# Optimization experiments

Measured on AMD Instinct MI355X. Metric: run time of the kernel, lower is better.

## Reference

```python
import jax, jax.numpy as jnp
import numpy as np

B, S, D, H = 2, 2048, 1024, 16
DK = D // H  # 64
THETA = 10000.0


def setup_inputs() -> dict:
    key = jax.random.key(0)
    ks = jax.random.split(key, 5)
    scale = 1.0 / np.sqrt(D)
    return {
        "x": jax.random.normal(ks[0], (B, S, D), dtype=jnp.float32),
        "Wq": jax.random.normal(ks[1], (D, D), dtype=jnp.float32) * scale,
        "Wk": jax.random.normal(ks[2], (D, D), dtype=jnp.float32) * scale,
        "Wv": jax.random.normal(ks[3], (D, D), dtype=jnp.float32) * scale,
        "Wo": jax.random.normal(ks[4], (D, D), dtype=jnp.float32) * scale,
    }


def _rope(t):
    # t: (B, H, S, DK); interleaved-pair rotary embedding with positions 0..S-1
    s = t.shape[-2]
    inv_freq = 1.0 / (THETA ** (jnp.arange(0, DK, 2, dtype=jnp.float32) / DK))  # (DK/2,)
    ang = jnp.arange(s, dtype=jnp.float32)[:, None] * inv_freq[None, :]  # (S, DK/2)
    cos, sin = jnp.cos(ang), jnp.sin(ang)
    x1 = t[..., 0::2]
    x2 = t[..., 1::2]
    r1 = x1 * cos - x2 * sin
    r2 = x1 * sin + x2 * cos
    return jnp.stack([r1, r2], axis=-1).reshape(t.shape)


def reference(x, Wq, Wk, Wv, Wo):
    # Projections (Linear: y = x @ W^T), split heads -> (B, H, S, DK)
    def proj(W):
        y = jnp.einsum('bsd,ed->bse', x, W)
        return y.reshape(B, S, H, DK).transpose(0, 2, 1, 3)

    Q = _rope(proj(Wq))
    K = _rope(proj(Wk))
    V = proj(Wv)

    scores = jnp.einsum('bhqd,bhkd->bhqk', Q, K)
    scores = jnp.clip(scores, -80.0, 80.0)
    causal = jnp.tril(jnp.ones((S, S), dtype=bool))  # (S, S)
    scores = jnp.where(causal, scores, -jnp.inf)
    weights = jax.nn.softmax(scores / np.sqrt(DK), axis=-1)
    att = jnp.einsum('bhqk,bhkd->bhqd', weights, V)
    att = att.transpose(0, 2, 1, 3).reshape(B, S, D)
    return jnp.einsum('bsd,ed->bse', att, Wo)
```

## Files before the change

### kernel.cpp

```cpp
#include <hip/hip_runtime.h>
#include <hip/hip_bf16.h>

#define B_  2
#define S_  2048
#define D_  1024
#define H_  16
#define DK_ 64
#define BH_ (B_*H_)
#define M_  (B_*S_)

typedef __attribute__((ext_vector_type(8))) short bf16x8;
typedef __attribute__((ext_vector_type(4))) float f32x4;

__device__ inline float bf2f(unsigned short u) {
    return __uint_as_float(((unsigned)u) << 16);
}
__device__ inline unsigned short f2bf(float f) {
    unsigned u = __float_as_uint(f);
    u += 0x7fffu + ((u >> 16) & 1u);
    return (unsigned short)(u >> 16);
}
__device__ inline unsigned short f2bf_hw(float f) {
    __hip_bfloat16 h = __float2bfloat16(f);
    return *reinterpret_cast<unsigned short*>(&h);
}
__device__ inline unsigned packbf2(float lo, float hi) {
    return (unsigned)f2bf_hw(lo) | ((unsigned)f2bf_hw(hi) << 16);
}

__device__ inline void gld16(const void* g, void* l) {
    __builtin_amdgcn_global_load_lds(
        (const __attribute__((address_space(1))) unsigned int*)g,
        (__attribute__((address_space(3))) unsigned int*)l, 16, 0, 0);
}

__global__ void cast_f32_to_bf16(const float* __restrict__ src,
                                 unsigned short* __restrict__ dst, int n) {
    int i = (blockIdx.x * blockDim.x + threadIdx.x) * 4;
    int stride = gridDim.x * blockDim.x * 4;
    for (int j = i; j < n; j += stride) {
        float4 v = *reinterpret_cast<const float4*>(src + j);
        ushort4 o;
        o.x = f2bf(v.x); o.y = f2bf(v.y); o.z = f2bf(v.z); o.w = f2bf(v.w);
        *reinterpret_cast<ushort4*>(dst + j) = o;
    }
}

__global__ void cast4_f32_to_bf16(const float* __restrict__ s0, const float* __restrict__ s1,
                                  const float* __restrict__ s2, const float* __restrict__ s3,
                                  unsigned short* __restrict__ d0, unsigned short* __restrict__ d1,
                                  unsigned short* __restrict__ d2, unsigned short* __restrict__ d3) {
    const float* s; unsigned short* d;
    switch (blockIdx.y) {
        case 0: s = s0; d = d0; break;
        case 1: s = s1; d = d1; break;
        case 2: s = s2; d = d2; break;
        default: s = s3; d = d3; break;
    }
    int j = (blockIdx.x * blockDim.x + threadIdx.x) * 4;
    float4 v = *reinterpret_cast<const float4*>(s + j);
    ushort4 o;
    o.x = f2bf(v.x); o.y = f2bf(v.y); o.z = f2bf(v.z); o.w = f2bf(v.w);
    *reinterpret_cast<ushort4*>(d + j) = o;
}

#define BMQ 128
#define BNQ 128

__global__ __launch_bounds__(256)
void gemm_qkv(const unsigned short* __restrict__ A, const unsigned short* __restrict__ Wcat,
              unsigned short* __restrict__ Qf, unsigned short* __restrict__ Kf,
              unsigned short* __restrict__ Vf) {
    __shared__ unsigned short As[BMQ * 64];
    __shared__ unsigned short Bs[BNQ * 64];
    const int K = D_;
    const int tid  = threadIdx.x;
    const int lane = tid & 63;
    const int wid  = tid >> 6;
    const int wm = wid & 1, wn = wid >> 1;
    const int m0 = blockIdx.y * BMQ, n0 = blockIdx.x * BNQ;
    const int g  = lane >> 4, cl = lane & 15;

    f32x4 acc[4][4];
#pragma unroll
    for (int i = 0; i < 4; i++)
#pragma unroll
        for (int j = 0; j < 4; j++) acc[i][j] = f32x4{0.f, 0.f, 0.f, 0.f};

    const int srow = tid >> 3;
    const unsigned short* Asrc[4];
    const unsigned short* Bsrc[4];
#pragma unroll
    for (int q = 0; q < 4; q++) {
        int row = srow + q * 32;
        Asrc[q] = A    + (long)(m0 + row) * K + (((tid & 7) ^ (srow & 7)) * 8);
        Bsrc[q] = Wcat + (long)(n0 + row) * K + (((tid & 7) ^ (srow & 7)) * 8);
    }

    for (int k0 = 0; k0 < K; k0 += 64) {
        __syncthreads();
#pragma unroll
        for (int q = 0; q < 4; q++) gld16(Asrc[q] + k0, As + tid * 8 + q * 2048);
#pragma unroll
        for (int q = 0; q < 4; q++) gld16(Bsrc[q] + k0, Bs + tid * 8 + q * 2048);
        __syncthreads();

#pragma unroll
        for (int kk = 0; kk < 2; kk++) {
            bf16x8 af[4], bfr[4];
#pragma unroll
            for (int i = 0; i < 4; i++) {
                int row = wm*64 + i*16 + cl;
                af[i]  = *reinterpret_cast<const bf16x8*>(As + row * 64 + (((kk*4 + g) ^ (cl & 7)) * 8));
            }
#pragma unroll
            for (int j = 0; j < 4; j++) {
                int row = wn*64 + j*16 + cl;
                bfr[j] = *reinterpret_cast<const bf16x8*>(Bs + row * 64 + (((kk*4 + g) ^ (cl & 7)) * 8));
            }
#pragma unroll
            for (int i = 0; i < 4; i++)
#pragma unroll
                for (int j = 0; j < 4; j++)
                    acc[i][j] = __builtin_amdgcn_mfma_f32_16x16x32_bf16(af[i], bfr[j], acc[i][j], 0, 0, 0);
        }
    }

    const int mat = n0 >> 10;
    if (mat < 2) {
        float invf[4];
#pragma unroll
        for (int jj = 0; jj < 4; jj++)
            invf[jj] = exp2f(-(float)(jj*8 + (cl >> 1)) * 0.4152410118569779f);
#pragma unroll
        for (int i = 0; i < 4; i++) {
#pragma unroll
            for (int jj = 0; jj < 4; jj++) {
                const int gcl = (n0 & 1023) + wn*64 + jj*16 + cl;
                const int hh = gcl >> 6;
                const int dk = jj*16 + cl;
#pragma unroll
                for (int rr = 0; rr < 4; rr++) {
                    int gr = m0 + wm*64 + i*16 + g*4 + rr;
                    int bb = gr >> 11, s = gr & (S_ - 1);
                    float v = acc[i][jj][rr];
                    float p = __shfl_xor(v, 1);
                    float ang = (float)s * invf[jj];
                    float sn = __sinf(ang), cs = __cosf(ang);
                    float r = (cl & 1) ? fmaf(v, cs, p * sn) : fmaf(v, cs, -p * sn);
                    long idx;
                    if (mat == 0) {
                        const int lane_p = (s & 15) | (((dk >> 3) & 3) << 4);
                        idx = ((long)(bb*H_ + hh) * 128 + (s >> 4)) * 1024
                            + (dk >> 5) * 512 + lane_p * 8 + (dk & 7);
                        Qf[idx] = f2bf_hw(r);
                    } else {
                        const int vv = s & 63;
                        const int ng = ((vv >> 5) << 1) | ((vv >> 2) & 1);
                        const int slot = ((vv & 31) >> 3) * 4 + (vv & 3);
                        const int lane_p = slot | (((dk >> 3) & 3) << 4);
                        idx = (((long)(bb*H_ + hh) * 32 + (s >> 6)) * 4 + ng) * 1024
                            + (dk >> 5) * 512 + lane_p * 8 + (dk & 7);
                        Kf[idx] = f2bf_hw(r);
                    }
                }
            }
        }
    } else {
#pragma unroll
        for (int i = 0; i < 4; i++) {
#pragma unroll
            for (int jj = 0; jj < 4; jj++) {
                const int gcl = (n0 & 1023) + wn*64 + jj*16 + cl;
                const int hh = gcl >> 6;
                const int sbase = m0 + wm*64 + i*16 + g*4;
                const int bb = sbase >> 11, s0l = sbase & (S_ - 1);
                const int lane_p = cl | (((s0l >> 3) & 3) << 4);
                const int e0 = s0l & 7;
                ushort4 o;
                o.x = f2bf_hw(acc[i][jj][0]); o.y = f2bf_hw(acc[i][jj][1]);
                o.z = f2bf_hw(acc[i][jj][2]); o.w = f2bf_hw(acc[i][jj][3]);
                long idx = ((long)(bb*H_ + hh) * 4 + jj) * 32768
                         + (long)(s0l >> 5) * 512 + lane_p * 8 + e0;
                *reinterpret_cast<ushort4*>(Vf + idx) = o;
            }
        }
    }
}

#define BM 64
#define BN 128

__global__ __launch_bounds__(256)
void gemm_out(const unsigned short* __restrict__ A, const unsigned short* __restrict__ Bw,
              float* __restrict__ Cf) {
    __shared__ unsigned short As[BM * 64];
    __shared__ unsigned short Bs[BN * 64];
    const int K = D_;
    const int tid  = threadIdx.x;
    const int lane = tid & 63;
    const int wid  = tid >> 6;
    const int wm = wid & 1, wn = wid >> 1;
    const int m0 = blockIdx.y * BM, n0 = blockIdx.x * BN;
    const int g  = lane >> 4, cl = lane & 15;

    f32x4 acc[2][4];
#pragma unroll
    for (int i = 0; i < 2; i++)
#pragma unroll
        for (int j = 0; j < 4; j++) acc[i][j] = f32x4{0.f, 0.f, 0.f, 0.f};

    const int srow = tid >> 3;
    const unsigned short* Asrc[2];
    const unsigned short* Bsrc[4];
#pragma unroll
    for (int q = 0; q < 2; q++) {
        int row = srow + q * 32;
        Asrc[q] = A + (long)(m0 + row) * K + (((tid & 7) ^ (srow & 7)) * 8);
    }
#pragma unroll
    for (int q = 0; q < 4; q++) {
        int row = srow + q * 32;
        Bsrc[q] = Bw + (long)(n0 + row) * K + (((tid & 7) ^ (srow & 7)) * 8);
    }

    for (int k0 = 0; k0 < K; k0 += 64) {
        __syncthreads();
#pragma unroll
        for (int q = 0; q < 2; q++) gld16(Asrc[q] + k0, As + tid * 8 + q * 2048);
#pragma unroll
        for (int q = 0; q < 4; q++) gld16(Bsrc[q] + k0, Bs + tid * 8 + q * 2048);
        __syncthreads();

#pragma unroll
        for (int kk = 0; kk < 2; kk++) {
            bf16x8 af[2], bfr[4];
#pragma unroll
            for (int i = 0; i < 2; i++) {
                int row = wm*32 + i*16 + cl;
                af[i]  = *reinterpret_cast<const bf16x8*>(As + row * 64 + (((kk*4 + g) ^ (cl & 7)) * 8));
            }
#pragma unroll
            for (int j = 0; j < 4; j++) {
                int row = wn*64 + j*16 + cl;
                bfr[j] = *reinterpret_cast<const bf16x8*>(Bs + row * 64 + (((kk*4 + g) ^ (cl & 7)) * 8));
            }
#pragma unroll
            for (int i = 0; i < 2; i++)
#pragma unroll
                for (int j = 0; j < 4; j++)
                    acc[i][j] = __builtin_amdgcn_mfma_f32_16x16x32_bf16(af[i], bfr[j], acc[i][j], 0, 0, 0);
        }
    }

#pragma unroll
    for (int i = 0; i < 2; i++)
#pragma unroll
        for (int j = 0; j < 4; j++)
#pragma unroll
            for (int rr = 0; rr < 4; rr++) {
                int gr = m0 + wm*32 + i*16 + g*4 + rr;
                int gc = n0 + wn*64 + j*16 + cl;
                Cf[(long)gr * D_ + gc] = acc[i][j][rr];
            }
}

#define WQ    32
#define KVBLK 64

__global__ __launch_bounds__(256)
void flash_attn(const unsigned short* __restrict__ Qf, const unsigned short* __restrict__ Kf,
                const unsigned short* __restrict__ Vf, unsigned short* __restrict__ Att) {
    __shared__ __align__(16) char smem[17408];
    const int tid  = threadIdx.x;
    const int lane = tid & 63;
    const int wid  = tid >> 6;
    const int g = lane >> 4, cl = lane & 15;
    const int bh = blockIdx.x & (BH_ - 1);
    const int pr = blockIdx.x >> 5;
    const int b = bh >> 4, h = bh & (H_ - 1);

    f32x4* Ol = reinterpret_cast<f32x4*>(smem);
    float* Ll = reinterpret_cast<float*>(smem + 16384);

    const unsigned short* Qb = Qf + (long)bh * 131072;
    const unsigned short* Kb = Kf + (long)bh * 131072;
    const unsigned short* Vb = Vf + (long)bh * 131072;

    const float RS = 0.125f * 1.44269504f;
    const float RB = -10.f * 1.44269504f;

    for (int half = 0; half < 2; half++) {
        const int qt = half ? (S_/WQ - 1 - pr) : pr;
        const int q0 = qt * WQ;
        const int nt = (q0 + WQ + KVBLK - 1) / KVBLK;

        bf16x8 aq[2][2];
#pragma unroll
        for (int m = 0; m < 2; m++)
#pragma unroll
            for (int c = 0; c < 2; c++)
                aq[m][c] = *reinterpret_cast<const bf16x8*>(Qb + ((q0 >> 4) + m) * 1024 + c * 512 + lane * 8);

        f32x4 o[2][4];
#pragma unroll
        for (int m = 0; m < 2; m++)
#pragma unroll
            for (int t = 0; t < 4; t++) o[m][t] = f32x4{0.f, 0.f, 0.f, 0.f};
        float lp[2] = {0.f, 0.f};

        for (int j = wid; j < nt; j += 4) {
            const int kv0 = j * KVBLK;
            bf16x8 bk[4][2];
#pragma unroll
            for (int n = 0; n < 4; n++)
#pragma unroll
                for (int c = 0; c < 2; c++)
                    bk[n][c] = *reinterpret_cast<const bf16x8*>(Kb + (j * 4 + n) * 1024 + c * 512 + lane * 8);
            f32x4 sc[2][4];
#pragma unroll
            for (int m = 0; m < 2; m++)
#pragma unroll
                for (int n = 0; n < 4; n++) {
                    f32x4 z = f32x4{0.f, 0.f, 0.f, 0.f};
                    z = __builtin_amdgcn_mfma_f32_16x16x32_bf16(bk[n][0], aq[m][0], z, 0, 0, 0);
                    z = __builtin_amdgcn_mfma_f32_16x16x32_bf16(bk[n][1], aq[m][1], z, 0, 0, 0);
                    sc[m][n] = z;
                }

            bf16x8 bv[4][2];
#pragma unroll
            for (int t = 0; t < 4; t++)
#pragma unroll
                for (int c = 0; c < 2; c++)
                    bv[t][c] = *reinterpret_cast<const bf16x8*>(Vb + (long)t * 32768 + ((kv0 >> 5) + c) * 512 + lane * 8);

            const bool diag = (kv0 + KVBLK - 1 > q0);
#pragma unroll
            for (int m = 0; m < 2; m++) {
                const int q = q0 + m*16 + cl;
                union { unsigned u[4]; bf16x8 v; } w0, w1;
#pragma unroll
                for (int n = 0; n < 4; n++) {
                    float p4[4];
#pragma unroll
                    for (int rr = 0; rr < 4; rr++) {
                        float u2 = fminf(fmaf(sc[m][n][rr], RS, RB), 0.f);
                        float pe = __builtin_amdgcn_exp2f(u2);
                        if (diag) {
                            const int kv = kv0 + ((n >> 1) << 5) + (g << 3) + ((n & 1) << 2) + rr;
                            if (kv > q) pe = 0.f;
                        }
                        p4[rr] = pe;
                    }
                    lp[m] += (p4[0] + p4[1]) + (p4[2] + p4[3]);
                    const unsigned lo = packbf2(p4[0], p4[1]);
                    const unsigned hi = packbf2(p4[2], p4[3]);
                    if (n == 0)      { w0.u[0] = lo; w0.u[1] = hi; }
                    else if (n == 1) { w0.u[2] = lo; w0.u[3] = hi; }
                    else if (n == 2) { w1.u[0] = lo; w1.u[1] = hi; }
                    else             { w1.u[2] = lo; w1.u[3] = hi; }
                }
#pragma unroll
                for (int t = 0; t < 4; t++) {
                    o[m][t] = __builtin_amdgcn_mfma_f32_16x16x32_bf16(w0.v, bv[t][0], o[m][t], 0, 0, 0);
                    o[m][t] = __builtin_amdgcn_mfma_f32_16x16x32_bf16(w1.v, bv[t][1], o[m][t], 0, 0, 0);
                }
            }
        }

        __syncthreads();
        if (wid == 1 || wid == 3) {
            const int slot = wid >> 1;
#pragma unroll
            for (int m = 0; m < 2; m++) {
#pragma unroll
                for (int t = 0; t < 4; t++)
                    Ol[(slot*8 + m*4 + t)*64 + lane] = o[m][t];
                Ll[(slot*2 + m)*64 + lane] = lp[m];
            }
        }
        __syncthreads();
        if (wid == 0 || wid == 2) {
            const int slot = wid >> 1;
#pragma unroll
            for (int m = 0; m < 2; m++) {
#pragma unroll
                for (int t = 0; t < 4; t++) {
                    f32x4 v = Ol[(slot*8 + m*4 + t)*64 + lane];
#pragma unroll
                    for (int rr = 0; rr < 4; rr++) o[m][t][rr] += v[rr];
                }
                lp[m] += Ll[(slot*2 + m)*64 + lane];
            }
        }
        __syncthreads();
        if (wid == 2) {
#pragma unroll
            for (int m = 0; m < 2; m++) {
#pragma unroll
                for (int t = 0; t < 4; t++)
                    Ol[(m*4 + t)*64 + lane] = o[m][t];
                Ll[m*64 + lane] = lp[m];
            }
        }
        __syncthreads();
        if (wid == 0) {
#pragma unroll
            for (int m = 0; m < 2; m++) {
#pragma unroll
                for (int t = 0; t < 4; t++) {
                    f32x4 v = Ol[(m*4 + t)*64 + lane];
#pragma unroll
                    for (int rr = 0; rr < 4; rr++) o[m][t][rr] += v[rr];
                }
                lp[m] += Ll[m*64 + lane];
                lp[m] += __shfl_xor(lp[m], 16);
                lp[m] += __shfl_xor(lp[m], 32);
            }
            float linv[2][4];
#pragma unroll
            for (int m = 0; m < 2; m++)
#pragma unroll
                for (int rr = 0; rr < 4; rr++)
                    linv[m][rr] = 1.0f / __shfl(lp[m], g*4 + rr);
#pragma unroll
            for (int m = 0; m < 2; m++)
#pragma unroll
                for (int t = 0; t < 4; t++)
#pragma unroll
                    for (int rr = 0; rr < 4; rr++) {
                        const int q = q0 + m*16 + g*4 + rr;
                        const int d = t*16 + cl;
                        Att[(long)(b * S_ + q) * D_ + h * DK_ + d] = f2bf_hw(o[m][t][rr] * linv[m][rr]);
                    }
        }
        __syncthreads();
    }
}

extern "C" void kernel_launch(void* const* d_in, const int* in_sizes, int n_in,
                              void* d_out, int out_size, void* d_ws, size_t ws_size,
                              hipStream_t stream) {
    const float* x  = (const float*)d_in[0];
    const float* Wq = (const float*)d_in[1];
    const float* Wk = (const float*)d_in[2];
    const float* Wv = (const float*)d_in[3];
    const float* Wo = (const float*)d_in[4];
    float* out = (float*)d_out;

    char* ws = (char*)d_ws;
    unsigned short* xb  = (unsigned short*)(ws);
    unsigned short* att = xb;
    unsigned short* WqB = (unsigned short*)(ws + (8  << 20));
    unsigned short* WkB = (unsigned short*)(ws + (10 << 20));
    unsigned short* WvB = (unsigned short*)(ws + (12 << 20));
    unsigned short* WoB = (unsigned short*)(ws + (14 << 20));
    unsigned short* Qf  = (unsigned short*)(ws + (16 << 20));
    unsigned short* Kf  = (unsigned short*)(ws + (24 << 20));
    unsigned short* Vf  = (unsigned short*)(ws + (32 << 20));

    const int nx = B_ * S_ * D_;
    cast_f32_to_bf16<<<4096, 256, 0, stream>>>(x, xb, nx);
    cast4_f32_to_bf16<<<dim3(1024, 4), 256, 0, stream>>>(Wq, Wk, Wv, Wo, WqB, WkB, WvB, WoB);

    dim3 qkvgrid(3 * D_ / BNQ, M_ / BMQ);
    gemm_qkv<<<qkvgrid, 256, 0, stream>>>(xb, WqB, Qf, Kf, Vf);

    flash_attn<<<(S_/WQ/2) * BH_, 256, 0, stream>>>(Qf, Kf, Vf, att);

    dim3 ogrid(D_ / BN, M_ / BM);
    gemm_out<<<ogrid, 256, 0, stream>>>(att, WoB, out);
}
```

Measured before the change: 117.2 us.

## Halve QKV GEMM M-tile and precompute RoPE sin/cos table

```diff
diff --git a/kernel.cpp b/kernel.cpp
--- a/kernel.cpp
+++ b/kernel.cpp
@@ -32,6 +32,15 @@
     __builtin_amdgcn_global_load_lds(
         (const __attribute__((address_space(1))) unsigned int*)g,
         (__attribute__((address_space(3))) unsigned int*)l, 16, 0, 0);
+}
+
+__global__ void rope_tab(float2* __restrict__ Tab) {
+    int idx = blockIdx.x * blockDim.x + threadIdx.x;
+    int s = idx >> 5, i = idx & 31;
+    float ang = (float)s * exp2f(-(float)i * 0.4152410118569779f);
+    float sn, cs;
+    sincosf(ang, &sn, &cs);
+    Tab[idx] = float2{cs, sn};
 }
 
 __global__ void cast_f32_to_bf16(const float* __restrict__ src,
@@ -64,53 +73,58 @@
     *reinterpret_cast<ushort4*>(d + j) = o;
 }
 
-#define BMQ 128
-#define BNQ 128
+#define BM 64
+#define BN 128
 
 __global__ __launch_bounds__(256)
 void gemm_qkv(const unsigned short* __restrict__ A, const unsigned short* __restrict__ Wcat,
+              const float2* __restrict__ Tab,
               unsigned short* __restrict__ Qf, unsigned short* __restrict__ Kf,
               unsigned short* __restrict__ Vf) {
-    __shared__ unsigned short As[BMQ * 64];
-    __shared__ unsigned short Bs[BNQ * 64];
+    __shared__ unsigned short As[BM * 64];
+    __shared__ unsigned short Bs[BN * 64];
     const int K = D_;
     const int tid  = threadIdx.x;
     const int lane = tid & 63;
     const int wid  = tid >> 6;
     const int wm = wid & 1, wn = wid >> 1;
-    const int m0 = blockIdx.y * BMQ, n0 = blockIdx.x * BNQ;
+    const int m0 = blockIdx.y * BM, n0 = blockIdx.x * BN;
     const int g  = lane >> 4, cl = lane & 15;
 
-    f32x4 acc[4][4];
-#pragma unroll
-    for (int i = 0; i < 4; i++)
+    f32x4 acc[2][4];
+#pragma unroll
+    for (int i = 0; i < 2; i++)
 #pragma unroll
         for (int j = 0; j < 4; j++) acc[i][j] = f32x4{0.f, 0.f, 0.f, 0.f};
 
     const int srow = tid >> 3;
-    const unsigned short* Asrc[4];
+    const unsigned short* Asrc[2];
     const unsigned short* Bsrc[4];
+#pragma unroll
+    for (int q = 0; q < 2; q++) {
+        int row = srow + q * 32;
+        Asrc[q] = A + (long)(m0 + row) * K + (((tid & 7) ^ (srow & 7)) * 8);
+    }
 #pragma unroll
     for (int q = 0; q < 4; q++) {
         int row = srow + q * 32;
-        Asrc[q] = A    + (long)(m0 + row) * K + (((tid & 7) ^ (srow & 7)) * 8);
         Bsrc[q] = Wcat + (long)(n0 + row) * K + (((tid & 7) ^ (srow & 7)) * 8);
     }
 
     for (int k0 = 0; k0 < K; k0 += 64) {
         __syncthreads();
 #pragma unroll
-        for (int q = 0; q < 4; q++) gld16(Asrc[q] + k0, As + tid * 8 + q * 2048);
+        for (int q = 0; q < 2; q++) gld16(Asrc[q] + k0, As + tid * 8 + q * 2048);
 #pragma unroll
         for (int q = 0; q < 4; q++) gld16(Bsrc[q] + k0, Bs + tid * 8 + q * 2048);
         __syncthreads();
 
 #pragma unroll
         for (int kk = 0; kk < 2; kk++) {
-            bf16x8 af[4], bfr[4];
-#pragma unroll
-            for (int i = 0; i < 4; i++) {
-                int row = wm*64 + i*16 + cl;
+            bf16x8 af[2], bfr[4];
+#pragma unroll
+            for (int i = 0; i < 2; i++) {
+                int row = wm*32 + i*16 + cl;
                 af[i]  = *reinterpret_cast<const bf16x8*>(As + row * 64 + (((kk*4 + g) ^ (cl & 7)) * 8));
             }
 #pragma unroll
@@ -119,7 +133,7 @@
                 bfr[j] = *reinterpret_cast<const bf16x8*>(Bs + row * 64 + (((kk*4 + g) ^ (cl & 7)) * 8));
             }
 #pragma unroll
-            for (int i = 0; i < 4; i++)
+            for (int i = 0; i < 2; i++)
 #pragma unroll
                 for (int j = 0; j < 4; j++)
                     acc[i][j] = __builtin_amdgcn_mfma_f32_16x16x32_bf16(af[i], bfr[j], acc[i][j], 0, 0, 0);
@@ -128,26 +142,22 @@
 
     const int mat = n0 >> 10;
     if (mat < 2) {
-        float invf[4];
-#pragma unroll
-        for (int jj = 0; jj < 4; jj++)
-            invf[jj] = exp2f(-(float)(jj*8 + (cl >> 1)) * 0.4152410118569779f);
-#pragma unroll
-        for (int i = 0; i < 4; i++) {
+#pragma unroll
+        for (int i = 0; i < 2; i++) {
 #pragma unroll
             for (int jj = 0; jj < 4; jj++) {
                 const int gcl = (n0 & 1023) + wn*64 + jj*16 + cl;
                 const int hh = gcl >> 6;
                 const int dk = jj*16 + cl;
+                const int ifr = jj*8 + (cl >> 1);
 #pragma unroll
                 for (int rr = 0; rr < 4; rr++) {
-                    int gr = m0 + wm*64 + i*16 + g*4 + rr;
+                    int gr = m0 + wm*32 + i*16 + g*4 + rr;
                     int bb = gr >> 11, s = gr & (S_ - 1);
                     float v = acc[i][jj][rr];
                     float p = __shfl_xor(v, 1);
-                    float ang = (float)s * invf[jj];
-                    float sn = __sinf(ang), cs = __cosf(ang);
-                    float r = (cl & 1) ? fmaf(v, cs, p * sn) : fmaf(v, cs, -p * sn);
+                    float2 t = Tab[s * 32 + ifr];
+                    float r = (cl & 1) ? fmaf(v, t.x, p * t.y) : fmaf(v, t.x, -p * t.y);
                     long idx;
                     if (mat == 0) {
                         const int lane_p = (s & 15) | (((dk >> 3) & 3) << 4);
@@ -168,12 +178,12 @@
         }
     } else {
 #pragma unroll
-        for (int i = 0; i < 4; i++) {
+        for (int i = 0; i < 2; i++) {
 #pragma unroll
             for (int jj = 0; jj < 4; jj++) {
                 const int gcl = (n0 & 1023) + wn*64 + jj*16 + cl;
                 const int hh = gcl >> 6;
-                const int sbase = m0 + wm*64 + i*16 + g*4;
+                const int sbase = m0 + wm*32 + i*16 + g*4;
                 const int bb = sbase >> 11, s0l = sbase & (S_ - 1);
                 const int lane_p = cl | (((s0l >> 3) & 3) << 4);
                 const int e0 = s0l & 7;
@@ -187,9 +197,6 @@
         }
     }
 }
-
-#define BM 64
-#define BN 128
 
 __global__ __launch_bounds__(256)
 void gemm_out(const unsigned short* __restrict__ A, const unsigned short* __restrict__ Bw,
@@ -460,12 +467,15 @@
     unsigned short* Kf  = (unsigned short*)(ws + (24 << 20));
     unsigned short* Vf  = (unsigned short*)(ws + (32 << 20));
 
+    float2* Tab = (float2*)d_out;
+
     const int nx = B_ * S_ * D_;
+    rope_tab<<<256, 256, 0, stream>>>(Tab);
     cast_f32_to_bf16<<<4096, 256, 0, stream>>>(x, xb, nx);
     cast4_f32_to_bf16<<<dim3(1024, 4), 256, 0, stream>>>(Wq, Wk, Wv, Wo, WqB, WkB, WvB, WoB);
 
-    dim3 qkvgrid(3 * D_ / BNQ, M_ / BMQ);
-    gemm_qkv<<<qkvgrid, 256, 0, stream>>>(xb, WqB, Qf, Kf, Vf);
+    dim3 qkvgrid(3 * D_ / BN, M_ / BM);
+    gemm_qkv<<<qkvgrid, 256, 0, stream>>>(xb, WqB, Tab, Qf, Kf, Vf);
 
     flash_attn<<<(S_/WQ/2) * BH_, 256, 0, stream>>>(Qf, Kf, Vf, att);
 
```

New measurement: 125.6 us. 1.07x slower.
